# Performance work log

Hardware: AMD Instinct MI355X
Metric: run time of the kernel (lower is better)

The kernel has to match this reference:

```python
import jax, jax.numpy as jnp
import numpy as np

HEADS = 16  # config.heads


def setup_inputs() -> dict:
    key = jax.random.key(0)
    k1, k2, k3, k4 = jax.random.split(key, 4)
    B, S, H = 2, 2048, 2048
    x = jax.random.normal(k1, (B, S, H), dtype=jnp.float32)
    w_qkv = jax.random.normal(k2, (H, 3 * H), dtype=jnp.float32) * 0.02
    b_qkv = jax.random.normal(k3, (3 * H,), dtype=jnp.float32) * 0.02
    w_o = jax.random.normal(k4, (H, H), dtype=jnp.float32) * 0.02
    return {"x": x, "w_qkv": w_qkv, "b_qkv": b_qkv, "w_o": w_o}


def reference(x, w_qkv, b_qkv, w_o):
    # pre_layer_norm=False path: plain linear QKV projection
    B, S, H = x.shape
    hd = H // HEADS  # head_size
    scale = 1.0 / jnp.sqrt(jnp.float32(hd))  # 1/norm_factor^2, use_mup=False
    qkv = x @ w_qkv + b_qkv  # [B, S, 3H]
    q, k, v = qkv[..., :H], qkv[..., H:2 * H], qkv[..., 2 * H:]

    def split_heads(t):  # [B,S,H] -> [B,heads,S,hd]
        return t.reshape(B, S, HEADS, hd).transpose(0, 2, 1, 3)

    qh, kh, vh = split_heads(q), split_heads(k), split_heads(v)
    # score_4d_matmul with triangular masking + scale
    scores = jnp.einsum('bhqd,bhkd->bhqk', qh, kh) * scale  # [B,h,S,S]
    causal = jnp.tril(jnp.ones((S, S), dtype=bool))
    scores = jnp.where(causal, scores, -jnp.inf)
    probs = jax.nn.softmax(scores, axis=-1)
    # context_4d_matmul -> merge heads back to [B,S,H]
    ctx = jnp.einsum('bhqk,bhkd->bhqd', probs, vh)
    ctx = ctx.transpose(0, 2, 1, 3).reshape(B, S, H)
    # vector_matmul with attn_ow (no bias in this path)
    out = ctx @ w_o
    return out
```

## Files before the change

kernel.cpp:

```cpp
#include <hip/hip_runtime.h>
#include <cstdint>
#include <cstddef>

typedef __attribute__((ext_vector_type(8))) short bf16x8;
typedef __attribute__((ext_vector_type(4))) float f32x4;
typedef __attribute__((ext_vector_type(4))) unsigned short ushort4_;

#define MFMA16(a, b, c) __builtin_amdgcn_mfma_f32_16x16x32_bf16((a), (b), (c), 0, 0, 0)

__device__ __forceinline__ unsigned short f2bf(float f) {
  union { float f; unsigned u; } c; c.f = f;
  unsigned r = c.u + 0x7fffu + ((c.u >> 16) & 1u);
  return (unsigned short)(r >> 16);
}

__device__ __forceinline__ void gl_lds16(const unsigned short* g, unsigned short* l) {
  __builtin_amdgcn_global_load_lds(
      (const __attribute__((address_space(1))) void*)g,
      (__attribute__((address_space(3))) void*)l, 16, 0, 0);
}

__global__ __launch_bounds__(256) void k_prep(const float* __restrict__ x,
                                              unsigned short* __restrict__ xb,
                                              const float* __restrict__ wqkv,
                                              unsigned short* __restrict__ wqkvT,
                                              const float* __restrict__ wo,
                                              unsigned short* __restrict__ woT) {
  __shared__ unsigned short t[64][65];
  const int blk = blockIdx.x;
  const int tid = threadIdx.x;
  if (blk < 8192) {
    int i = blk * 256 + tid;
    float4 v = reinterpret_cast<const float4*>(x)[i];
    ushort4_ o;
    o.x = f2bf(v.x); o.y = f2bf(v.y); o.z = f2bf(v.z); o.w = f2bf(v.w);
    reinterpret_cast<ushort4_*>(xb)[i] = o;
    return;
  }
  const float* W;
  unsigned short* WT;
  int n0, k0, N;
  if (blk < 11264) {
    int local = blk - 8192;
    W = wqkv; WT = wqkvT; N = 6144;
    n0 = (local % 96) * 64; k0 = (local / 96) * 64;
  } else {
    int local = blk - 11264;
    W = wo; WT = woT; N = 2048;
    n0 = (local % 32) * 64; k0 = (local / 32) * 64;
  }
#pragma unroll
  for (int i = 0; i < 16; i++) {
    int li = tid + i * 256;
    int kk = li >> 6, nn = li & 63;
    t[kk][nn] = f2bf(W[(size_t)(k0 + kk) * N + (n0 + nn)]);
  }
  __syncthreads();
#pragma unroll
  for (int i = 0; i < 16; i++) {
    int li = tid + i * 256;
    int nn = li >> 6, kk = li & 63;
    WT[(size_t)(n0 + nn) * 2048 + (k0 + kk)] = t[kk][nn];
  }
}

template <int MODE>
__global__ __launch_bounds__(256) void k_gemm(const unsigned short* __restrict__ A,
                                              const unsigned short* __restrict__ Bt,
                                              const float* __restrict__ bias,
                                              unsigned short* __restrict__ qb,
                                              unsigned short* __restrict__ kb,
                                              unsigned short* __restrict__ vtb,
                                              float* __restrict__ outp) {
  __shared__ __align__(16) unsigned short As[128 * 64];
  __shared__ __align__(16) unsigned short Bs[128 * 64];
  const int tid = threadIdx.x;
  const int lane = tid & 63, wid = tid >> 6;
  const int quad = lane >> 4, l16 = lane & 15;
  const int wm = wid >> 1, wn = wid & 1;
  const int m0 = blockIdx.y * 128, n0 = blockIdx.x * 128;

  f32x4 acc[4][4];
#pragma unroll
  for (int i = 0; i < 4; i++)
#pragma unroll
    for (int j = 0; j < 4; j++) {
      f32x4 z = {0.f, 0.f, 0.f, 0.f};
      acc[i][j] = z;
    }

  for (int k0 = 0; k0 < 2048; k0 += 64) {
    __syncthreads();
#pragma unroll
    for (int i = 0; i < 4; i++) {
      int slotbase = wid * 64 + i * 256;
      int slot = slotbase + lane;
      int row = slot >> 3, chs = slot & 7, gch = chs ^ (row & 7);
      gl_lds16(A + (size_t)(m0 + row) * 2048 + k0 + gch * 8, &As[slotbase * 8]);
      gl_lds16(Bt + (size_t)(n0 + row) * 2048 + k0 + gch * 8, &Bs[slotbase * 8]);
    }
    __syncthreads();
#pragma unroll
    for (int kc = 0; kc < 2; kc++) {
      bf16x8 af[4], bfr[4];
#pragma unroll
      for (int mt = 0; mt < 4; mt++) {
        int r = wm * 64 + mt * 16 + l16;
        int ch = kc * 4 + quad;
        af[mt] = *reinterpret_cast<const bf16x8*>(&As[r * 64 + ((ch ^ (r & 7)) * 8)]);
      }
#pragma unroll
      for (int nt = 0; nt < 4; nt++) {
        int r = wn * 64 + nt * 16 + l16;
        int ch = kc * 4 + quad;
        bfr[nt] = *reinterpret_cast<const bf16x8*>(&Bs[r * 64 + ((ch ^ (r & 7)) * 8)]);
      }
#pragma unroll
      for (int mt = 0; mt < 4; mt++)
#pragma unroll
        for (int nt = 0; nt < 4; nt++)
          acc[mt][nt] = MFMA16(af[mt], bfr[nt], acc[mt][nt]);
    }
  }

  const int mbase = m0 + wm * 64;
  const int nbase = n0 + wn * 64;
  if (MODE == 0) {
#pragma unroll
    for (int nt = 0; nt < 4; nt++) {
      int n = nbase + nt * 16 + l16;
      float bv = bias[n];
      int seg = n >> 11;
      int h = (n >> 7) & 15;
      int d = n & 127;
#pragma unroll
      for (int mt = 0; mt < 4; mt++) {
        int mrow = mbase + mt * 16 + quad * 4;
        int b = mrow >> 11, s = mrow & 2047;
        if (seg == 2) {
          ushort4_ pk;
          pk.x = f2bf(acc[mt][nt][0] + bv);
          pk.y = f2bf(acc[mt][nt][1] + bv);
          pk.z = f2bf(acc[mt][nt][2] + bv);
          pk.w = f2bf(acc[mt][nt][3] + bv);
          *reinterpret_cast<ushort4_*>(vtb + ((size_t)(b * 16 + h) * 128 + d) * 2048 + s) = pk;
        } else {
          unsigned short* dst = (seg == 0 ? qb : kb);
          size_t base = (size_t)(b * 16 + h) * 2048;
#pragma unroll
          for (int rg = 0; rg < 4; rg++)
            dst[(base + (s + rg)) * 128 + d] = f2bf(acc[mt][nt][rg] + bv);
        }
      }
    }
  } else {
#pragma unroll
    for (int nt = 0; nt < 4; nt++) {
      int n = nbase + nt * 16 + l16;
#pragma unroll
      for (int mt = 0; mt < 4; mt++) {
        int mrow = mbase + mt * 16 + quad * 4;
#pragma unroll
        for (int rg = 0; rg < 4; rg++)
          outp[(size_t)(mrow + rg) * 2048 + n] = acc[mt][nt][rg];
      }
    }
  }
}

__global__ __launch_bounds__(256, 2) void k_attn(const unsigned short* __restrict__ qb,
                                                 const unsigned short* __restrict__ kb,
                                                 const unsigned short* __restrict__ vtb,
                                                 unsigned short* __restrict__ ctx) {
  __shared__ __align__(16) unsigned short Ks[2][64 * 128];
  __shared__ __align__(16) unsigned short Vs[2][128 * 64];
  __shared__ __align__(16) unsigned short Ps[128 * 64];
  const int bx = blockIdx.x;
  const int g = (bx & 1) ? (15 - (bx >> 1)) : (bx >> 1);
  const int qt = (blockIdx.y < 16) ? g : (15 - g);
  const int bh = blockIdx.y;
  const int tid = threadIdx.x;
  const int lane = tid & 63, w = tid >> 6;
  const int quad = lane >> 4, l16 = lane & 15;
  const int qbase = qt * 128;
  const unsigned short* Qh = qb + (size_t)bh * 2048 * 128;
  const unsigned short* Kh = kb + (size_t)bh * 2048 * 128;
  const unsigned short* Vh = vtb + (size_t)bh * 128 * 2048;

  const int q_lo = qbase + w * 32;
  const int nkv = 2 * qt + 2;
  const float sl2 = 0.12751741f;

  bf16x8 qf[2][4];
#pragma unroll
  for (int half = 0; half < 2; half++)
#pragma unroll
    for (int kc = 0; kc < 4; kc++)
      qf[half][kc] = *reinterpret_cast<const bf16x8*>(
          Qh + (size_t)(q_lo + half * 16 + l16) * 128 + kc * 32 + quad * 8);

  f32x4 o[2][8];
#pragma unroll
  for (int half = 0; half < 2; half++)
#pragma unroll
    for (int dt = 0; dt < 8; dt++) {
      f32x4 z = {0.f, 0.f, 0.f, 0.f};
      o[half][dt] = z;
    }
  float m_run[2] = {-1e30f, -1e30f}, l_run[2] = {0.f, 0.f};

  auto stage = [&](int kvb, int bsel) {
    unsigned short* Kd = &Ks[bsel][0];
    unsigned short* Vd = &Vs[bsel][0];
#pragma unroll
    for (int i = 0; i < 4; i++) {
      int slotbase = i * 256 + w * 64;
      int slot = slotbase + lane;
      int rowk = slot >> 4, chk = (slot & 15) ^ (rowk & 7);
      gl_lds16(Kh + (size_t)(kvb + rowk) * 128 + chk * 8, Kd + slotbase * 8);
      int rowv = slot >> 3, chv = (slot & 7) ^ (rowv & 7);
      gl_lds16(Vh + (size_t)rowv * 2048 + kvb + chv * 8, Vd + slotbase * 8);
    }
  };

  stage(0, 0);

  for (int kv = 0; kv < nkv; kv++) {
    const int kvb = kv * 64;
    const int cur = kv & 1;
    asm volatile("s_waitcnt vmcnt(0)" ::: "memory");
    asm volatile("s_barrier" ::: "memory");
    if (kv + 1 < nkv) stage(kvb + 64, cur ^ 1);
    if (kvb > q_lo + 31) continue;

    const unsigned short* Kc = &Ks[cur][0];
    const unsigned short* Vc = &Vs[cur][0];

    f32x4 sacc[2][4];
#pragma unroll
    for (int half = 0; half < 2; half++)
#pragma unroll
      for (int nt = 0; nt < 4; nt++) {
        f32x4 z = {0.f, 0.f, 0.f, 0.f};
        sacc[half][nt] = z;
      }
#pragma unroll
    for (int kc = 0; kc < 4; kc++) {
#pragma unroll
      for (int nt = 0; nt < 4; nt++) {
        int r = nt * 16 + l16, ch = kc * 4 + quad;
        bf16x8 kf = *reinterpret_cast<const bf16x8*>(&Kc[r * 128 + ((ch ^ (r & 7)) * 8)]);
        sacc[0][nt] = MFMA16(kf, qf[0][kc], sacc[0][nt]);
        sacc[1][nt] = MFMA16(kf, qf[1][kc], sacc[1][nt]);
      }
    }

    const bool needmask = (kvb + 63) > q_lo;
#pragma unroll
    for (int half = 0; half < 2; half++) {
      const int qabs = q_lo + half * 16 + l16;
      float tmax = -1e30f;
#pragma unroll
      for (int nt = 0; nt < 4; nt++)
#pragma unroll
        for (int rg = 0; rg < 4; rg++) {
          float v = sacc[half][nt][rg] * sl2;
          if (needmask && (kvb + nt * 16 + quad * 4 + rg) > qabs) v = -1e30f;
          sacc[half][nt][rg] = v;
          tmax = fmaxf(tmax, v);
        }
      tmax = fmaxf(tmax, __shfl_xor(tmax, 16));
      tmax = fmaxf(tmax, __shfl_xor(tmax, 32));
      float mnew = fmaxf(m_run[half], tmax);
      float alpha = exp2f(m_run[half] - mnew);
      m_run[half] = mnew;
      float rsum = 0.f;
#pragma unroll
      for (int nt = 0; nt < 4; nt++)
#pragma unroll
        for (int rg = 0; rg < 4; rg++) {
          float p = exp2f(sacc[half][nt][rg] - mnew);
          sacc[half][nt][rg] = p;
          rsum += p;
        }
      rsum += __shfl_xor(rsum, 16);
      rsum += __shfl_xor(rsum, 32);
      l_run[half] = l_run[half] * alpha + rsum;
#pragma unroll
      for (int dt = 0; dt < 8; dt++)
#pragma unroll
        for (int rg = 0; rg < 4; rg++) o[half][dt][rg] *= alpha;

#pragma unroll
      for (int nt = 0; nt < 4; nt++) {
        ushort4_ pk;
        pk.x = f2bf(sacc[half][nt][0]);
        pk.y = f2bf(sacc[half][nt][1]);
        pk.z = f2bf(sacc[half][nt][2]);
        pk.w = f2bf(sacc[half][nt][3]);
        int chunk = nt * 2 + (quad >> 1);
        *reinterpret_cast<ushort4_*>(
            &Ps[(w * 32 + half * 16 + l16) * 64 + ((chunk ^ (l16 & 7)) * 8) +
                (quad & 1) * 4]) = pk;
      }
    }
    asm volatile("s_waitcnt lgkmcnt(0)" ::: "memory");

#pragma unroll
    for (int kc = 0; kc < 2; kc++) {
      int chunkr = kc * 4 + quad;
      bf16x8 pf0 = *reinterpret_cast<const bf16x8*>(
          &Ps[(w * 32 + l16) * 64 + ((chunkr ^ (l16 & 7)) * 8)]);
      bf16x8 pf1 = *reinterpret_cast<const bf16x8*>(
          &Ps[(w * 32 + 16 + l16) * 64 + ((chunkr ^ (l16 & 7)) * 8)]);
#pragma unroll
      for (int dt = 0; dt < 8; dt++) {
        int r = dt * 16 + l16, ch = kc * 4 + quad;
        bf16x8 vf = *reinterpret_cast<const bf16x8*>(&Vc[r * 64 + ((ch ^ (r & 7)) * 8)]);
        o[0][dt] = MFMA16(vf, pf0, o[0][dt]);
        o[1][dt] = MFMA16(vf, pf1, o[1][dt]);
      }
    }
  }

  const int b = bh >> 4, h = bh & 15;
#pragma unroll
  for (int half = 0; half < 2; half++) {
    const float inv = 1.f / l_run[half];
    const int s = q_lo + half * 16 + l16;
#pragma unroll
    for (int dt = 0; dt < 8; dt++) {
      int d0 = dt * 16 + quad * 4;
      ushort4_ pk;
      pk.x = f2bf(o[half][dt][0] * inv);
      pk.y = f2bf(o[half][dt][1] * inv);
      pk.z = f2bf(o[half][dt][2] * inv);
      pk.w = f2bf(o[half][dt][3] * inv);
      *reinterpret_cast<ushort4_*>(
          &ctx[((size_t)b * 2048 + s) * 2048 + h * 128 + d0]) = pk;
    }
  }
}

extern "C" void kernel_launch(void* const* d_in, const int* in_sizes, int n_in,
                              void* d_out, int out_size, void* d_ws, size_t ws_size,
                              hipStream_t stream) {
  const float* x = (const float*)d_in[0];
  const float* w_qkv = (const float*)d_in[1];
  const float* b_qkv = (const float*)d_in[2];
  const float* w_o = (const float*)d_in[3];
  float* outp = (float*)d_out;

  unsigned short* ws = (unsigned short*)d_ws;
  unsigned short* xb    = ws;
  unsigned short* wqkvT = xb + 8388608;
  unsigned short* woT   = wqkvT + 12582912;
  unsigned short* qbuf  = woT + 4194304;
  unsigned short* kbuf  = qbuf + 8388608;
  unsigned short* vtbuf = kbuf + 8388608;
  unsigned short* ctxb  = vtbuf + 8388608;

  k_prep<<<12288, 256, 0, stream>>>(x, xb, w_qkv, wqkvT, w_o, woT);
  k_gemm<0><<<dim3(48, 32), 256, 0, stream>>>(xb, wqkvT, b_qkv, qbuf, kbuf, vtbuf, nullptr);
  k_attn<<<dim3(16, 32), 256, 0, stream>>>(qbuf, kbuf, vtbuf, ctxb);
  k_gemm<1><<<dim3(16, 32), 256, 0, stream>>>(ctxb, woT, nullptr, nullptr, nullptr, nullptr, outp);
}
```

Before: 392.5 us.

## Replace QKV GEMM with 256x256 tiled, 8-wave, phase-pipelined kernel

Adds a new QKV projection GEMM that uses 256x256 output tiles with 512 threads, double-buffered swizzled LDS filled by direct global-to-LDS loads, and a four-phase schedule. Each phase interleaves fragment loads, prefetch of the next tile and MFMA bursts, with barriers and raised wave priority around the MFMAs. Blocks are remapped in an XCD-aware swizzle. The goal is more data reuse per tile and better overlap of memory with compute than the old 128-tile GEMM. In exchange it uses 128 KB of LDS per block and adds many barriers, which can limit occupancy.

```diff
diff --git a/kernel.cpp b/kernel.cpp
--- a/kernel.cpp
+++ b/kernel.cpp
@@ -163,6 +163,183 @@
 #pragma unroll
         for (int rg = 0; rg < 4; rg++)
           outp[(size_t)(mrow + rg) * 2048 + n] = acc[mt][nt][rg];
+      }
+    }
+  }
+}
+
+template <int MH>
+__device__ __forceinline__ void lda_frag(const unsigned short* Asb, int wm, int quad,
+                                         int l16, bf16x8 (&a)[4][2]) {
+#pragma unroll
+  for (int mi = 0; mi < 4; mi++)
+#pragma unroll
+    for (int kcc = 0; kcc < 2; kcc++) {
+      int r = wm * 128 + MH * 64 + mi * 16 + l16;
+      int ch = kcc * 4 + quad;
+      a[mi][kcc] = *reinterpret_cast<const bf16x8*>(&Asb[r * 64 + ((ch ^ (r & 7)) * 8)]);
+    }
+}
+
+template <int NH>
+__device__ __forceinline__ void ldb_frag(const unsigned short* Bsb, int wn, int quad,
+                                         int l16, bf16x8 (&b)[2][2][2]) {
+#pragma unroll
+  for (int ni = 0; ni < 2; ni++)
+#pragma unroll
+    for (int kcc = 0; kcc < 2; kcc++) {
+      int r = wn * 64 + NH * 32 + ni * 16 + l16;
+      int ch = kcc * 4 + quad;
+      b[NH][ni][kcc] = *reinterpret_cast<const bf16x8*>(&Bsb[r * 64 + ((ch ^ (r & 7)) * 8)]);
+    }
+}
+
+template <int MH, int NH>
+__device__ __forceinline__ void phase_mfma(f32x4 (&acc)[8][4], const bf16x8 (&a)[4][2],
+                                           const bf16x8 (&b)[2][2][2]) {
+  __builtin_amdgcn_s_setprio(1);
+#pragma unroll
+  for (int kcc = 0; kcc < 2; kcc++)
+#pragma unroll
+    for (int mi = 0; mi < 4; mi++)
+#pragma unroll
+      for (int ni = 0; ni < 2; ni++)
+        acc[MH * 4 + mi][NH * 2 + ni] =
+            MFMA16(a[mi][kcc], b[NH][ni][kcc], acc[MH * 4 + mi][NH * 2 + ni]);
+  __builtin_amdgcn_s_setprio(0);
+}
+
+#define G2_BAR asm volatile("s_barrier" ::: "memory")
+#define G2_LGKM0                                      \
+  asm volatile("s_waitcnt lgkmcnt(0)" ::: "memory"); \
+  __builtin_amdgcn_sched_barrier(0)
+#define G2_VM4 asm volatile("s_waitcnt vmcnt(4)" ::: "memory")
+
+__global__ __launch_bounds__(512, 2) void k_gemm2(const unsigned short* __restrict__ A,
+                                                  const unsigned short* __restrict__ Bt,
+                                                  const float* __restrict__ bias,
+                                                  unsigned short* __restrict__ qb,
+                                                  unsigned short* __restrict__ kb,
+                                                  unsigned short* __restrict__ vtb,
+                                                  int ntn) {
+  __shared__ __align__(16) unsigned short As[2][256 * 64];
+  __shared__ __align__(16) unsigned short Bs[2][256 * 64];
+  const int tid = threadIdx.x;
+  const int lane = tid & 63, wid = tid >> 6;
+  const int quad = lane >> 4, l16 = lane & 15;
+  const int wm = wid >> 2, wn = wid & 3;
+
+  const int nwg = gridDim.x, bid = blockIdx.x;
+  const int cpx = nwg >> 3;
+  const int swz = (bid & 7) * cpx + (bid >> 3);
+  const int tm = swz / ntn, tn = swz % ntn;
+  const int m0 = tm * 256, n0 = tn * 256;
+
+  f32x4 acc[8][4];
+#pragma unroll
+  for (int i = 0; i < 8; i++)
+#pragma unroll
+    for (int j = 0; j < 4; j++) {
+      f32x4 z = {0.f, 0.f, 0.f, 0.f};
+      acc[i][j] = z;
+    }
+
+  auto stA = [&](int tsrc, int buf, int rbase) {
+#pragma unroll
+    for (int s = 0; s < 2; s++) {
+      int slotbase = s * 512 + wid * 64;
+      int slot = slotbase + lane;
+      int row = rbase + (slot >> 3);
+      int ch = (slot & 7) ^ (row & 7);
+      gl_lds16(A + (size_t)(m0 + row) * 2048 + tsrc * 64 + ch * 8,
+               &As[buf][rbase * 64 + slotbase * 8]);
+    }
+  };
+  auto stB = [&](int tsrc, int buf, int rbase) {
+#pragma unroll
+    for (int s = 0; s < 2; s++) {
+      int slotbase = s * 512 + wid * 64;
+      int slot = slotbase + lane;
+      int row = rbase + (slot >> 3);
+      int ch = (slot & 7) ^ (row & 7);
+      gl_lds16(Bt + (size_t)(n0 + row) * 2048 + tsrc * 64 + ch * 8,
+               &Bs[buf][rbase * 64 + slotbase * 8]);
+    }
+  };
+
+  bf16x8 a[4][2];
+  bf16x8 b[2][2][2];
+
+  stA(0, 0, 0); stA(0, 0, 128);
+  stB(0, 0, 0); stB(0, 0, 128);
+  stB(1, 1, 0); stB(1, 1, 128);
+  G2_VM4;
+  G2_BAR;
+
+  const int nt = 32;
+  for (int t = 0; t < nt; t++) {
+    const int buf = t & 1;
+    const unsigned short* Asb = &As[buf][0];
+    const unsigned short* Bsb = &Bs[buf][0];
+    const int tA = (t + 1 < nt) ? t + 1 : t;
+    const int tB = (t + 2 < nt) ? t + 2 : t;
+
+    lda_frag<0>(Asb, wm, quad, l16, a);
+    ldb_frag<0>(Bsb, wn, quad, l16, b);
+    stA(tA, buf ^ 1, 0);
+    G2_BAR;
+    G2_LGKM0;
+    phase_mfma<0, 0>(acc, a, b);
+    G2_BAR;
+
+    ldb_frag<1>(Bsb, wn, quad, l16, b);
+    stA(tA, buf ^ 1, 128);
+    G2_BAR;
+    G2_LGKM0;
+    phase_mfma<0, 1>(acc, a, b);
+    G2_BAR;
+
+    lda_frag<1>(Asb, wm, quad, l16, a);
+    stB(tB, buf, 0);
+    G2_BAR;
+    G2_LGKM0;
+    phase_mfma<1, 0>(acc, a, b);
+    G2_BAR;
+
+    stB(tB, buf, 128);
+    G2_BAR;
+    phase_mfma<1, 1>(acc, a, b);
+    G2_VM4;
+    G2_BAR;
+  }
+  asm volatile("s_waitcnt vmcnt(0)" ::: "memory");
+
+  const int mbase = m0 + wm * 128;
+  const int nbase = n0 + wn * 64;
+#pragma unroll
+  for (int ntf = 0; ntf < 4; ntf++) {
+    int n = nbase + ntf * 16 + l16;
+    float bv = bias[n];
+    int seg = n >> 11;
+    int h = (n >> 7) & 15;
+    int d = n & 127;
+#pragma unroll
+    for (int mt = 0; mt < 8; mt++) {
+      int mrow = mbase + mt * 16 + quad * 4;
+      int bb = mrow >> 11, s = mrow & 2047;
+      if (seg == 2) {
+        ushort4_ pk;
+        pk.x = f2bf(acc[mt][ntf][0] + bv);
+        pk.y = f2bf(acc[mt][ntf][1] + bv);
+        pk.z = f2bf(acc[mt][ntf][2] + bv);
+        pk.w = f2bf(acc[mt][ntf][3] + bv);
+        *reinterpret_cast<ushort4_*>(vtb + ((size_t)(bb * 16 + h) * 128 + d) * 2048 + s) = pk;
+      } else {
+        unsigned short* dst = (seg == 0 ? qb : kb);
+        size_t base = (size_t)(bb * 16 + h) * 2048;
+#pragma unroll
+        for (int rg = 0; rg < 4; rg++)
+          dst[(base + (s + rg)) * 128 + d] = f2bf(acc[mt][ntf][rg] + bv);
       }
     }
   }
@@ -361,7 +538,7 @@
   unsigned short* ctxb  = vtbuf + 8388608;
 
   k_prep<<<12288, 256, 0, stream>>>(x, xb, w_qkv, wqkvT, w_o, woT);
-  k_gemm<0><<<dim3(48, 32), 256, 0, stream>>>(xb, wqkvT, b_qkv, qbuf, kbuf, vtbuf, nullptr);
+  k_gemm2<<<384, 512, 0, stream>>>(xb, wqkvT, b_qkv, qbuf, kbuf, vtbuf, 24);
   k_attn<<<dim3(16, 32), 256, 0, stream>>>(qbuf, kbuf, vtbuf, ctxb);
   k_gemm<1><<<dim3(16, 32), 256, 0, stream>>>(ctxb, woT, nullptr, nullptr, nullptr, nullptr, outp);
 }
```

Result: slower. 418.0 us (+6.5%).
